# Performance work log

Hardware: AMD Instinct MI355X
Metric: run time of the kernel (lower is better)

Reference implementation:

```python
import jax, jax.numpy as jnp
import numpy as np

B, SQ, HID, NH, PAST = 8, 16, 1024, 16, 4096
DH = HID // NH
ROPE_BASE = 10000.0


def _rope(x, pos):
    # rotate-half RoPE applied over the full hidden dim (as in the module, rope
    # is built with hidden_size and applied before the head split)
    half = x.shape[-1] // 2
    inv_freq = 1.0 / (ROPE_BASE ** (jnp.arange(half, dtype=jnp.float32) / half))
    ang = pos[..., None].astype(jnp.float32) * inv_freq  # [B, S, half]
    cos, sin = jnp.cos(ang), jnp.sin(ang)
    x1, x2 = x[..., :half], x[..., half:]
    return jnp.concatenate([x1 * cos - x2 * sin, x2 * cos + x1 * sin], axis=-1).astype(x.dtype)


def setup_inputs() -> dict:
    key = jax.random.key(0)
    ks = jax.random.split(key, 16)
    s = 1.0 / np.sqrt(HID)
    return {
        "hidden_state": jax.random.normal(ks[0], (B, SQ, HID), jnp.float32),
        "attention_mask": jnp.zeros((B, SQ, SQ), jnp.float32),
        "past_key": jax.random.normal(ks[1], (B, NH, PAST, DH), jnp.float32),
        "past_value": jax.random.normal(ks[2], (B, NH, PAST, DH), jnp.float32),
        "position_ids": jax.random.randint(ks[3], (B, SQ), 0, 4200, jnp.int32),
        "Wq": jax.random.normal(ks[4], (HID, HID), jnp.float32) * s,
        "bq": jnp.zeros((HID,), jnp.float32),
        "Wk": jax.random.normal(ks[5], (HID, HID), jnp.float32) * s,
        "bk": jnp.zeros((HID,), jnp.float32),
        "Wv": jax.random.normal(ks[6], (HID, HID), jnp.float32) * s,
        "bv": jnp.zeros((HID,), jnp.float32),
        "Wo": jax.random.normal(ks[7], (HID, HID), jnp.float32) * s,
        "bo": jnp.zeros((HID,), jnp.float32),
    }


def reference(hidden_state, attention_mask, past_key, past_value, position_ids,
              Wq, bq, Wk, bk, Wv, bv, Wo, bo):
    b, sq, hid = hidden_state.shape
    nh = NH
    dh = hid // nh

    q = hidden_state @ Wq + bq
    k = hidden_state @ Wk + bk
    v = hidden_state @ Wv + bv

    q = _rope(q, position_ids)
    k = _rope(k, position_ids)

    # split heads -> [B, H, S, Dh]
    q = q.reshape(b, sq, nh, dh).transpose(0, 2, 1, 3)
    k = k.reshape(b, sq, nh, dh).transpose(0, 2, 1, 3)
    v = v.reshape(b, sq, nh, dh).transpose(0, 2, 1, 3)

    # KV-cache concat along the key/seq dim
    new_key = jnp.concatenate((past_key, k), axis=2)      # [B, H, Skv, Dh]
    new_value = jnp.concatenate((past_value, v), axis=2)
    skv_past = past_key.shape[2]
    mask = jnp.concatenate(
        (jnp.zeros((b, sq, skv_past), attention_mask.dtype), attention_mask), axis=2)

    scale = 1.0 / jnp.sqrt(jnp.asarray(dh, q.dtype))
    scores = jnp.einsum("bhqd,bhkd->bhqk", q, new_key) * scale + mask[:, None]
    probs = jax.nn.softmax(scores, axis=-1)
    ctx = jnp.einsum("bhqk,bhkd->bhqd", probs, new_value)  # [B, H, Sq, Dh]

    out = ctx.transpose(0, 2, 1, 3).reshape(b, sq, hid) @ Wo + bo
    return (out, new_key, new_value)
```

## Files before the change

### kernel.cpp

```cpp
#include <hip/hip_runtime.h>
#include <math.h>

#define BB   8
#define SQ   16
#define HIDD 1024
#define NHD  16
#define PAST 4096
#define DH   64
#define SKV  (PAST + SQ)
#define NTOK (BB * SQ)

__global__ __launch_bounds__(256) void gemm3(
    const float* __restrict__ A,
    const float* __restrict__ W0, const float* __restrict__ W1, const float* __restrict__ W2,
    const float* __restrict__ b0, const float* __restrict__ b1, const float* __restrict__ b2,
    float* __restrict__ O0, float* __restrict__ O1, float* __restrict__ O2)
{
    const int nt   = blockIdx.x;
    const int mt   = blockIdx.y;
    const int wsel = nt >> 4;
    const int col0 = (nt & 15) * 64;
    const int m0   = mt * 32;
    const float* W    = (wsel == 0) ? W0 : (wsel == 1) ? W1 : W2;
    const float* bias = (wsel == 0) ? b0 : (wsel == 1) ? b1 : b2;
    float*       Out  = (wsel == 0) ? O0 : (wsel == 1) ? O1 : O2;

    __shared__ float As[32][33];
    __shared__ float Bs[32][64];

    const int t    = threadIdx.x;
    const int tm   = t >> 4;
    const int tn   = t & 15;
    const int arow = t >> 3;
    const int acol = (t & 7) << 2;
    const int brow = t >> 4;
    const int bcol = (t & 15) << 2;

    float acc0[4] = {0.f,0.f,0.f,0.f};
    float acc1[4] = {0.f,0.f,0.f,0.f};

    for (int k0 = 0; k0 < HIDD; k0 += 32) {
        __syncthreads();
        float4 a4 = *(const float4*)(A + (size_t)(m0 + arow) * HIDD + k0 + acol);
        As[arow][acol+0] = a4.x; As[arow][acol+1] = a4.y;
        As[arow][acol+2] = a4.z; As[arow][acol+3] = a4.w;
        *(float4*)(&Bs[brow][bcol]) =
            *(const float4*)(W + (size_t)(k0 + brow) * HIDD + col0 + bcol);
        *(float4*)(&Bs[brow + 16][bcol]) =
            *(const float4*)(W + (size_t)(k0 + brow + 16) * HIDD + col0 + bcol);
        __syncthreads();
        #pragma unroll
        for (int kk = 0; kk < 32; ++kk) {
            const float  a0 = As[2*tm][kk];
            const float  a1 = As[2*tm + 1][kk];
            const float4 b4 = *(const float4*)(&Bs[kk][tn << 2]);
            acc0[0] += a0*b4.x; acc0[1] += a0*b4.y; acc0[2] += a0*b4.z; acc0[3] += a0*b4.w;
            acc1[0] += a1*b4.x; acc1[1] += a1*b4.y; acc1[2] += a1*b4.z; acc1[3] += a1*b4.w;
        }
    }
    const float4 bb = *(const float4*)(bias + col0 + (tn << 2));
    float* o0 = Out + (size_t)(m0 + 2*tm) * HIDD + col0 + (tn << 2);
    float* o1 = o0 + HIDD;
    o0[0] = acc0[0] + bb.x; o0[1] = acc0[1] + bb.y; o0[2] = acc0[2] + bb.z; o0[3] = acc0[3] + bb.w;
    o1[0] = acc1[0] + bb.x; o1[1] = acc1[1] + bb.y; o1[2] = acc1[2] + bb.z; o1[3] = acc1[3] + bb.w;
}

__global__ __launch_bounds__(256) void rope_scatter(
    const float* __restrict__ qr, const float* __restrict__ kr, const float* __restrict__ vr,
    const int* __restrict__ pos_ids,
    float* __restrict__ Qh, float* __restrict__ nk, float* __restrict__ nv)
{
    const int tok = blockIdx.x;
    const int b   = tok >> 4;
    const int s   = tok & 15;
    const float pos = (float)pos_ids[tok];
    const size_t rq = (size_t)tok * HIDD;
    for (int i = threadIdx.x; i < 512; i += 256) {
        const float inv = expf((float)i * (-9.210340371976184f / 512.0f));
        const float ang = pos * inv;
        const float c  = cosf(ang);
        const float sn = sinf(ang);
        const int h1 = i >> 6, d = i & 63;
        const int h2 = h1 + 8;
        float x1, x2;
        x1 = qr[rq + i]; x2 = qr[rq + i + 512];
        Qh[((size_t)(b*NHD + h1)*SQ + s)*DH + d] = x1*c - x2*sn;
        Qh[((size_t)(b*NHD + h2)*SQ + s)*DH + d] = x2*c + x1*sn;
        x1 = kr[rq + i]; x2 = kr[rq + i + 512];
        nk[((size_t)(b*NHD + h1)*SKV + PAST + s)*DH + d] = x1*c - x2*sn;
        nk[((size_t)(b*NHD + h2)*SKV + PAST + s)*DH + d] = x2*c + x1*sn;
        x1 = vr[rq + i]; x2 = vr[rq + i + 512];
        nv[((size_t)(b*NHD + h1)*SKV + PAST + s)*DH + d] = x1;
        nv[((size_t)(b*NHD + h2)*SKV + PAST + s)*DH + d] = x2;
    }
}

__global__ __launch_bounds__(256) void attn_partial(
    const float* __restrict__ pk, const float* __restrict__ pv,
    const float* __restrict__ Qh, const float* __restrict__ amask,
    float* __restrict__ nk, float* __restrict__ nv,
    float* __restrict__ pc, float* __restrict__ pm, float* __restrict__ pl)
{
    const int chunk = blockIdx.x;
    const int bh    = blockIdx.y;
    const int b     = bh >> 4;
    const int t     = threadIdx.x;
    const int w     = t >> 6;
    const int lane  = t & 63;
    const int qq    = lane >> 4;
    const int d4    = lane & 15;

    __shared__ float  Qs[SQ * DH];
    __shared__ float4 Ks[64 * 16];
    __shared__ float  Vs[64 * DH];
    __shared__ float4 Ps[4 * 64];

    {
        const int q = t >> 4, i = t & 15;
        float4 q4 = *(const float4*)(Qh + ((size_t)bh * SQ + q) * DH + 4*i);
        q4.x *= 0.125f; q4.y *= 0.125f; q4.z *= 0.125f; q4.w *= 0.125f;
        *(float4*)(&Qs[q * DH + 4*i]) = q4;
    }

    float m_r[4], l_r[4];
    #pragma unroll
    for (int q = 0; q < 4; ++q) { m_r[q] = -3.0e38f; l_r[q] = 0.0f; }
    float4 ctx = make_float4(0.f, 0.f, 0.f, 0.f);

    const int ntiles = (chunk == 7) ? 9 : 8;
    for (int tile = 0; tile < ntiles; ++tile) {
        __syncthreads();
        if (tile < 8) {
            const int k0 = chunk * 512 + tile * 64;
            #pragma unroll
            for (int p = 0; p < 4; ++p) {
                const int c = t + 256 * p;
                const int j = c >> 4, i = c & 15;
                const size_t po = ((size_t)bh * PAST + k0 + j) * DH + 4*i;
                const size_t no = ((size_t)bh * SKV  + k0 + j) * DH + 4*i;
                const float4 k4 = *(const float4*)(pk + po);
                *(float4*)(nk + no) = k4;
                Ks[j * 16 + (i ^ (j & 7))] = k4;
                const float4 v4 = *(const float4*)(pv + po);
                *(float4*)(nv + no) = v4;
                *(float4*)(&Vs[j * DH + 4*i]) = v4;
            }
        } else {
            const int j = t >> 4, i = t & 15;
            const size_t no = ((size_t)bh * SKV + PAST + j) * DH + 4*i;
            Ks[j * 16 + (i ^ (j & 7))] = *(const float4*)(nk + no);
            *(float4*)(&Vs[j * DH + 4*i]) = *(const float4*)(nv + no);
        }
        __syncthreads();

        const int jcount = (tile < 8) ? 64 : 16;

        float s[4];
        {
            float4 acc[4];
            #pragma unroll
            for (int q = 0; q < 4; ++q) acc[q] = make_float4(0.f,0.f,0.f,0.f);
            if (lane < jcount) {
                #pragma unroll
                for (int i = 0; i < 16; ++i) {
                    const float4 k4 = Ks[lane * 16 + (i ^ (lane & 7))];
                    #pragma unroll
                    for (int q = 0; q < 4; ++q) {
                        const float4 q4 = *(const float4*)(&Qs[(4*w + q) * DH + 4*i]);
                        acc[q].x += k4.x * q4.x; acc[q].y += k4.y * q4.y;
                        acc[q].z += k4.z * q4.z; acc[q].w += k4.w * q4.w;
                    }
                }
            }
            #pragma unroll
            for (int q = 0; q < 4; ++q)
                s[q] = (lane < jcount) ? (acc[q].x + acc[q].y + acc[q].z + acc[q].w)
                                       : -3.0e38f;
        }
        if (tile == 8 && lane < 16) {
            #pragma unroll
            for (int q = 0; q < 4; ++q)
                s[q] += amask[((size_t)b * SQ + 4*w + q) * SQ + lane];
        }

        float alpha[4], pjv[4];
        #pragma unroll
        for (int q = 0; q < 4; ++q) {
            float mx = s[q];
            #pragma unroll
            for (int off = 1; off < 64; off <<= 1)
                mx = fmaxf(mx, __shfl_xor(mx, off, 64));
            const float mnew = fmaxf(m_r[q], mx);
            alpha[q] = __expf(m_r[q] - mnew);
            const float p = __expf(s[q] - mnew);
            pjv[q] = p;
            float ps = p;
            #pragma unroll
            for (int off = 1; off < 64; off <<= 1)
                ps += __shfl_xor(ps, off, 64);
            l_r[q] = l_r[q] * alpha[q] + ps;
            m_r[q] = mnew;
        }
        {
            float4 pw;
            pw.x = pjv[0]; pw.y = pjv[1]; pw.z = pjv[2]; pw.w = pjv[3];
            Ps[w * 64 + lane] = pw;
        }

        const float asel = (qq == 0) ? alpha[0] : (qq == 1) ? alpha[1]
                         : (qq == 2) ? alpha[2] : alpha[3];
        ctx.x *= asel; ctx.y *= asel; ctx.z *= asel; ctx.w *= asel;

        const float* Pf = (const float*)&Ps[w * 64];
        for (int j = 0; j < jcount; ++j) {
            const float  p  = Pf[4*j + qq];
            const float4 v4 = *(const float4*)(&Vs[j * DH + 4*d4]);
            ctx.x += p * v4.x; ctx.y += p * v4.y; ctx.z += p * v4.z; ctx.w += p * v4.w;
        }
    }

    const int blk = bh * 8 + chunk;
    const int qg  = 4*w + qq;
    *(float4*)(pc + (size_t)blk * 1024 + qg * DH + 4*d4) = ctx;
    if (d4 == 0) {
        const float msel = (qq == 0) ? m_r[0] : (qq == 1) ? m_r[1] : (qq == 2) ? m_r[2] : m_r[3];
        const float lsel = (qq == 0) ? l_r[0] : (qq == 1) ? l_r[1] : (qq == 2) ? l_r[2] : l_r[3];
        pm[blk * 16 + qg] = msel;
        pl[blk * 16 + qg] = lsel;
    }
}

__global__ __launch_bounds__(256) void attn_reduce(
    const float* __restrict__ pc, const float* __restrict__ pm,
    const float* __restrict__ pl, float* __restrict__ ctxw)
{
    const int bh = blockIdx.x;
    const int b  = bh >> 4, h = bh & 15;
    const int t  = threadIdx.x;
    __shared__ float mg[SQ], li[SQ];
    if (t < SQ) {
        float m = -3.0e38f;
        #pragma unroll
        for (int c = 0; c < 8; ++c) m = fmaxf(m, pm[(bh*8 + c) * 16 + t]);
        float L = 0.f;
        #pragma unroll
        for (int c = 0; c < 8; ++c)
            L += pl[(bh*8 + c) * 16 + t] * __expf(pm[(bh*8 + c) * 16 + t] - m);
        mg[t] = m; li[t] = 1.0f / L;
    }
    __syncthreads();
    #pragma unroll
    for (int r = 0; r < 4; ++r) {
        const int idx = t + 256 * r;
        const int q = idx >> 6, d = idx & 63;
        float acc = 0.f;
        #pragma unroll
        for (int c = 0; c < 8; ++c)
            acc += pc[(size_t)(bh*8 + c) * 1024 + idx]
                 * __expf(pm[(bh*8 + c) * 16 + q] - mg[q]);
        ctxw[((size_t)(b*SQ + q) * NHD + h) * DH + d] = acc * li[q];
    }
}

extern "C" void kernel_launch(void* const* d_in, const int* in_sizes, int n_in,
                              void* d_out, int out_size, void* d_ws, size_t ws_size,
                              hipStream_t stream)
{
    const float* hidden = (const float*)d_in[0];
    const float* amask  = (const float*)d_in[1];
    const float* past_k = (const float*)d_in[2];
    const float* past_v = (const float*)d_in[3];
    const int*   pos    = (const int*)  d_in[4];
    const float* Wq = (const float*)d_in[5];  const float* bq = (const float*)d_in[6];
    const float* Wk = (const float*)d_in[7];  const float* bk = (const float*)d_in[8];
    const float* Wv = (const float*)d_in[9];  const float* bv = (const float*)d_in[10];
    const float* Wo = (const float*)d_in[11]; const float* bo = (const float*)d_in[12];

    float* out = (float*)d_out;
    float* nk  = out + (size_t)NTOK * HIDD;
    float* nv  = nk + (size_t)BB * NHD * SKV * DH;

    float* ws     = (float*)d_ws;
    float* q_raw  = ws;
    float* k_raw  = q_raw + 131072;
    float* v_raw  = k_raw + 131072;
    float* Qh     = v_raw + 131072;
    float* pc     = Qh    + 131072;
    float* pm     = pc    + 1024 * 1024;
    float* pl     = pm    + 1024 * 16;
    float* ctxw   = pl    + 1024 * 16;

    gemm3<<<dim3(48, 4), 256, 0, stream>>>(hidden, Wq, Wk, Wv, bq, bk, bv,
                                           q_raw, k_raw, v_raw);
    rope_scatter<<<NTOK, 256, 0, stream>>>(q_raw, k_raw, v_raw, pos, Qh, nk, nv);
    attn_partial<<<dim3(8, 128), 256, 0, stream>>>(past_k, past_v, Qh, amask,
                                                   nk, nv, pc, pm, pl);
    attn_reduce<<<128, 256, 0, stream>>>(pc, pm, pl, ctxw);
    gemm3<<<dim3(16, 4), 256, 0, stream>>>(ctxw, Wo, Wo, Wo, bo, bo, bo,
                                           out, out, out);
}
```

Measured before the change: 581.9 us.

## Prefetch next tiles into registers, use fast sincos, vectorize PV loop, precompute reduce weights

The GEMM and attention kernels now load the next K/V or A/W tile into registers while the current tile is being computed, so global-load latency overlaps with compute. RoPE switches to fast __expf and __sincosf intrinsics, which may lose some accuracy for large angles. The probability buffer is laid out per query so the PV loop can read four probabilities as one float4 and process four keys per iteration. The reduce kernel computes the per-chunk exponential weights once in shared memory instead of recomputing them per element. Register pressure goes up because of the prefetch buffers.

Measured after the change: 600.7 us. 1.03x slower.

```diff
diff --git a/kernel.cpp b/kernel.cpp
--- a/kernel.cpp
+++ b/kernel.cpp
@@ -39,15 +39,21 @@
     float acc0[4] = {0.f,0.f,0.f,0.f};
     float acc1[4] = {0.f,0.f,0.f,0.f};
 
+    float4 ra  = *(const float4*)(A + (size_t)(m0 + arow) * HIDD + acol);
+    float4 rb0 = *(const float4*)(W + (size_t)brow        * HIDD + col0 + bcol);
+    float4 rb1 = *(const float4*)(W + (size_t)(brow + 16) * HIDD + col0 + bcol);
+
     for (int k0 = 0; k0 < HIDD; k0 += 32) {
         __syncthreads();
-        float4 a4 = *(const float4*)(A + (size_t)(m0 + arow) * HIDD + k0 + acol);
-        As[arow][acol+0] = a4.x; As[arow][acol+1] = a4.y;
-        As[arow][acol+2] = a4.z; As[arow][acol+3] = a4.w;
-        *(float4*)(&Bs[brow][bcol]) =
-            *(const float4*)(W + (size_t)(k0 + brow) * HIDD + col0 + bcol);
-        *(float4*)(&Bs[brow + 16][bcol]) =
-            *(const float4*)(W + (size_t)(k0 + brow + 16) * HIDD + col0 + bcol);
+        As[arow][acol+0] = ra.x; As[arow][acol+1] = ra.y;
+        As[arow][acol+2] = ra.z; As[arow][acol+3] = ra.w;
+        *(float4*)(&Bs[brow][bcol])      = rb0;
+        *(float4*)(&Bs[brow + 16][bcol]) = rb1;
+        if (k0 + 32 < HIDD) {
+            ra  = *(const float4*)(A + (size_t)(m0 + arow) * HIDD + k0 + 32 + acol);
+            rb0 = *(const float4*)(W + (size_t)(k0 + 32 + brow) * HIDD + col0 + bcol);
+            rb1 = *(const float4*)(W + (size_t)(k0 + 48 + brow) * HIDD + col0 + bcol);
+        }
         __syncthreads();
         #pragma unroll
         for (int kk = 0; kk < 32; ++kk) {
@@ -76,10 +82,10 @@
     const float pos = (float)pos_ids[tok];
     const size_t rq = (size_t)tok * HIDD;
     for (int i = threadIdx.x; i < 512; i += 256) {
-        const float inv = expf((float)i * (-9.210340371976184f / 512.0f));
+        const float inv = __expf((float)i * (-9.210340371976184f / 512.0f));
         const float ang = pos * inv;
-        const float c  = cosf(ang);
-        const float sn = sinf(ang);
+        float c, sn;
+        __sincosf(ang, &sn, &c);
         const int h1 = i >> 6, d = i & 63;
         const int h2 = h1 + 8;
         float x1, x2;
@@ -113,7 +119,23 @@
     __shared__ float  Qs[SQ * DH];
     __shared__ float4 Ks[64 * 16];
     __shared__ float  Vs[64 * DH];
-    __shared__ float4 Ps[4 * 64];
+    __shared__ float  Ps2[4][4][64];
+
+    const int j0 = t >> 4;
+    const int i0 = t & 15;
+    const size_t pbase = (size_t)bh * PAST * DH;
+    const size_t nbase = (size_t)bh * SKV  * DH;
+
+    float4 ka[4], va[4];
+    {
+        const int k0 = chunk * 512;
+        #pragma unroll
+        for (int p = 0; p < 4; ++p) {
+            const size_t po = pbase + (size_t)(k0 + j0 + 16*p) * DH + 4*i0;
+            ka[p] = *(const float4*)(pk + po);
+            va[p] = *(const float4*)(pv + po);
+        }
+    }
 
     {
         const int q = t >> 4, i = t & 15;
@@ -134,22 +156,26 @@
             const int k0 = chunk * 512 + tile * 64;
             #pragma unroll
             for (int p = 0; p < 4; ++p) {
-                const int c = t + 256 * p;
-                const int j = c >> 4, i = c & 15;
-                const size_t po = ((size_t)bh * PAST + k0 + j) * DH + 4*i;
-                const size_t no = ((size_t)bh * SKV  + k0 + j) * DH + 4*i;
-                const float4 k4 = *(const float4*)(pk + po);
-                *(float4*)(nk + no) = k4;
-                Ks[j * 16 + (i ^ (j & 7))] = k4;
-                const float4 v4 = *(const float4*)(pv + po);
-                *(float4*)(nv + no) = v4;
-                *(float4*)(&Vs[j * DH + 4*i]) = v4;
+                const int j = j0 + 16*p;
+                const size_t no = nbase + (size_t)(k0 + j) * DH + 4*i0;
+                Ks[j * 16 + (i0 ^ (j & 7))] = ka[p];
+                *(float4*)(&Vs[j * DH + 4*i0]) = va[p];
+                *(float4*)(nk + no) = ka[p];
+                *(float4*)(nv + no) = va[p];
+            }
+            if (tile < 7) {
+                const int k1 = chunk * 512 + (tile + 1) * 64;
+                #pragma unroll
+                for (int p = 0; p < 4; ++p) {
+                    const size_t po = pbase + (size_t)(k1 + j0 + 16*p) * DH + 4*i0;
+                    ka[p] = *(const float4*)(pk + po);
+                    va[p] = *(const float4*)(pv + po);
+                }
             }
         } else {
-            const int j = t >> 4, i = t & 15;
-            const size_t no = ((size_t)bh * SKV + PAST + j) * DH + 4*i;
-            Ks[j * 16 + (i ^ (j & 7))] = *(const float4*)(nk + no);
-            *(float4*)(&Vs[j * DH + 4*i]) = *(const float4*)(nv + no);
+            const size_t no = nbase + (size_t)(PAST + j0) * DH + 4*i0;
+            Ks[j0 * 16 + (i0 ^ (j0 & 7))] = *(const float4*)(nk + no);
+            *(float4*)(&Vs[j0 * DH + 4*i0]) = *(const float4*)(nv + no);
         }
         __syncthreads();
 
@@ -201,21 +227,26 @@
             l_r[q] = l_r[q] * alpha[q] + ps;
             m_r[q] = mnew;
         }
-        {
-            float4 pw;
-            pw.x = pjv[0]; pw.y = pjv[1]; pw.z = pjv[2]; pw.w = pjv[3];
-            Ps[w * 64 + lane] = pw;
-        }
+        #pragma unroll
+        for (int q = 0; q < 4; ++q)
+            Ps2[w][q][lane] = pjv[q];
 
         const float asel = (qq == 0) ? alpha[0] : (qq == 1) ? alpha[1]
                          : (qq == 2) ? alpha[2] : alpha[3];
         ctx.x *= asel; ctx.y *= asel; ctx.z *= asel; ctx.w *= asel;
 
-        const float* Pf = (const float*)&Ps[w * 64];
-        for (int j = 0; j < jcount; ++j) {
-            const float  p  = Pf[4*j + qq];
-            const float4 v4 = *(const float4*)(&Vs[j * DH + 4*d4]);
-            ctx.x += p * v4.x; ctx.y += p * v4.y; ctx.z += p * v4.z; ctx.w += p * v4.w;
+        const float* Pq = &Ps2[w][0][0] + qq * 64;
+        const int j4 = jcount >> 2;
+        for (int jj = 0; jj < j4; ++jj) {
+            const float4 p4 = *(const float4*)(Pq + 4*jj);
+            const float4 v0 = *(const float4*)(&Vs[(4*jj + 0) * DH + 4*d4]);
+            const float4 v1 = *(const float4*)(&Vs[(4*jj + 1) * DH + 4*d4]);
+            const float4 v2 = *(const float4*)(&Vs[(4*jj + 2) * DH + 4*d4]);
+            const float4 v3 = *(const float4*)(&Vs[(4*jj + 3) * DH + 4*d4]);
+            ctx.x += p4.x*v0.x; ctx.y += p4.x*v0.y; ctx.z += p4.x*v0.z; ctx.w += p4.x*v0.w;
+            ctx.x += p4.y*v1.x; ctx.y += p4.y*v1.y; ctx.z += p4.y*v1.z; ctx.w += p4.y*v1.w;
+            ctx.x += p4.z*v2.x; ctx.y += p4.z*v2.y; ctx.z += p4.z*v2.z; ctx.w += p4.z*v2.w;
+            ctx.x += p4.w*v3.x; ctx.y += p4.w*v3.y; ctx.z += p4.w*v3.z; ctx.w += p4.w*v3.w;
         }
     }
 
@@ -237,16 +268,20 @@
     const int bh = blockIdx.x;
     const int b  = bh >> 4, h = bh & 15;
     const int t  = threadIdx.x;
-    __shared__ float mg[SQ], li[SQ];
+    __shared__ float wgt[8][SQ];
+    __shared__ float li[SQ];
     if (t < SQ) {
         float m = -3.0e38f;
         #pragma unroll
         for (int c = 0; c < 8; ++c) m = fmaxf(m, pm[(bh*8 + c) * 16 + t]);
         float L = 0.f;
         #pragma unroll
-        for (int c = 0; c < 8; ++c)
-            L += pl[(bh*8 + c) * 16 + t] * __expf(pm[(bh*8 + c) * 16 + t] - m);
-        mg[t] = m; li[t] = 1.0f / L;
+        for (int c = 0; c < 8; ++c) {
+            const float e = __expf(pm[(bh*8 + c) * 16 + t] - m);
+            L += pl[(bh*8 + c) * 16 + t] * e;
+            wgt[c][t] = e;
+        }
+        li[t] = 1.0f / L;
     }
     __syncthreads();
     #pragma unroll
@@ -256,8 +291,7 @@
         float acc = 0.f;
         #pragma unroll
         for (int c = 0; c < 8; ++c)
-            acc += pc[(size_t)(bh*8 + c) * 1024 + idx]
-                 * __expf(pm[(bh*8 + c) * 16 + q] - mg[q]);
+            acc += pc[(size_t)(bh*8 + c) * 1024 + idx] * wgt[c][q];
         ctxw[((size_t)(b*SQ + q) * NHD + h) * DH + d] = acc * li[q];
     }
 }
```
